# Kernel optimization log

Measured on AMD Instinct MI355X. Metric: run time of the kernel, lower is better.

## Reference

```python
import jax, jax.numpy as jnp
import numpy as np

N_NODES = 100000
N_EDGES = 1600000
D_IN, D_HID, D_OUT = 512, 256, 32


def setup_inputs() -> dict:
    key = jax.random.key(0)
    ks = jax.random.split(key, 8)
    features = jax.random.normal(ks[0], (N_NODES, D_IN), dtype=jnp.float32)
    A_data = jax.random.uniform(ks[1], (N_EDGES,), dtype=jnp.float32)
    A_row = jax.random.randint(ks[2], (N_EDGES,), 0, N_NODES, dtype=jnp.int32)
    A_col = jax.random.randint(ks[3], (N_EDGES,), 0, N_NODES, dtype=jnp.int32)
    # MLP params (glorot-ish scaling)
    W1 = jax.random.normal(ks[4], (D_IN, D_HID), dtype=jnp.float32) * (1.0 / np.sqrt(D_IN))
    b1 = jnp.zeros((D_HID,), dtype=jnp.float32)
    W2 = jax.random.normal(ks[5], (D_HID, D_OUT), dtype=jnp.float32) * (1.0 / np.sqrt(D_HID))
    b2 = jnp.zeros((D_OUT,), dtype=jnp.float32)
    return {"features": features, "A_data": A_data, "W1": W1, "b1": b1,
            "W2": W2, "b2": b2, "A_row": A_row, "A_col": A_col}


def reference(features, A_data, W1, b1, W2, b2, A_row, A_col):
    # head_transform: 2-layer MLP (is_training=False -> dropout identity)
    h = jax.nn.relu(features @ W1 + b1)          # [N, D_HID]
    X = h @ W2 + b2                              # [N, D_OUT]
    # propagator dropout: rate=0.0 / eval mode -> identity on A
    # sparse COO A @ X: gather columns, scale by edge values, scatter-add to rows
    msgs = A_data[:, None] * X[A_col]            # [E, D_OUT]
    out = jax.ops.segment_sum(msgs, A_row, num_segments=N_NODES)  # [N, D_OUT]
    return out
```

## Files before the change

### kernel.cpp

```cpp
#include <hip/hip_runtime.h>
#include <hip/hip_bf16.h>

typedef __bf16 bf16;
typedef __attribute__((ext_vector_type(8))) __bf16 bf16x8;
typedef __attribute__((ext_vector_type(4))) float f32x4;

constexpr int D_IN  = 512;
constexpr int D_HID = 256;
constexpr int D_OUT = 32;
constexpr int BM = 64;
constexpr int BK = 64;
constexpr int HCP = 40;
constexpr int SCAN_VPT  = 8;
constexpr int SCAN_SPAN = 2048;
constexpr int NSLICE = 8;

#define GLOBAL_AS(p) ((const __attribute__((address_space(1))) void*)(p))
#define LDS_AS(p)    ((__attribute__((address_space(3))) void*)(p))

__global__ __launch_bounds__(256) void prep_kernel(
    const float* __restrict__ W1, const float* __restrict__ W2,
    bf16* __restrict__ W1T, bf16* __restrict__ W2T)
{
    int idx = blockIdx.x * 256 + threadIdx.x;
    if (idx < D_IN * D_HID) {
        int k = idx / D_HID, n = idx % D_HID;
        W1T[n * D_IN + k] = (bf16)W1[idx];
    }
    int j = idx - D_IN * D_HID;
    if (j >= 0 && j < D_HID * D_OUT) {
        int k = j / D_OUT, n = j % D_OUT;
        W2T[n * D_HID + k] = (bf16)W2[j];
    }
}

__global__ __launch_bounds__(256) void fused_mlp_kernel(
    const float* __restrict__ feat,
    const bf16* __restrict__ W1T, const bf16* __restrict__ W2T,
    const float* __restrict__ b1, const float* __restrict__ b2,
    float* __restrict__ X, int N)
{
    __shared__ __align__(16) char smem[D_HID * BK * sizeof(bf16)];
    bf16* Bsm = (bf16*)smem;
    bf16* Hc  = (bf16*)smem;

    const int tid  = threadIdx.x;
    const int wave = tid >> 6;
    const int lane = tid & 63;
    const int ln   = lane & 15;
    const int q    = lane >> 4;
    const int mw   = wave * 16;
    const int r0   = blockIdx.x * BM;

    f32x4 acc[16] = {};

    const long arow = (long)min(r0 + mw + ln, N - 1);
    const float* asrc = feat + arow * D_IN + q * 8;

    for (int k0 = 0; k0 < D_IN; k0 += BK) {
        #pragma unroll
        for (int i = 0; i < 8; ++i) {
            int c  = i * 256 + wave * 64 + lane;
            int sl = (c & 7) ^ ((c >> 3) & 7);
            const bf16* gsrc = W1T + ((c >> 3) * D_IN + k0 + sl * 8);
            bf16* lbase = Bsm + (i * 256 + wave * 64) * 8;
            __builtin_amdgcn_global_load_lds(GLOBAL_AS(gsrc), LDS_AS(lbase), 16, 0, 0);
        }

        bf16x8 af0, af1;
        {
            float4 f0 = *(const float4*)(asrc + k0);
            float4 f1 = *(const float4*)(asrc + k0 + 4);
            af0[0] = (bf16)f0.x; af0[1] = (bf16)f0.y; af0[2] = (bf16)f0.z; af0[3] = (bf16)f0.w;
            af0[4] = (bf16)f1.x; af0[5] = (bf16)f1.y; af0[6] = (bf16)f1.z; af0[7] = (bf16)f1.w;
            float4 f2 = *(const float4*)(asrc + k0 + 32);
            float4 f3 = *(const float4*)(asrc + k0 + 36);
            af1[0] = (bf16)f2.x; af1[1] = (bf16)f2.y; af1[2] = (bf16)f2.z; af1[3] = (bf16)f2.w;
            af1[4] = (bf16)f3.x; af1[5] = (bf16)f3.y; af1[6] = (bf16)f3.z; af1[7] = (bf16)f3.w;
        }

        __syncthreads();

        {
            const int psl0 = (0 * 4 + q) ^ (ln & 7);
            #pragma unroll
            for (int t = 0; t < 16; ++t) {
                bf16x8 bfv = *(const bf16x8*)&Bsm[(t * 16 + ln) * BK + psl0 * 8];
                acc[t] = __builtin_amdgcn_mfma_f32_16x16x32_bf16(af0, bfv, acc[t], 0, 0, 0);
            }
            const int psl1 = (1 * 4 + q) ^ (ln & 7);
            #pragma unroll
            for (int t = 0; t < 16; ++t) {
                bf16x8 bfv = *(const bf16x8*)&Bsm[(t * 16 + ln) * BK + psl1 * 8];
                acc[t] = __builtin_amdgcn_mfma_f32_16x16x32_bf16(af1, bfv, acc[t], 0, 0, 0);
            }
        }
        __syncthreads();
    }

    f32x4 acc2[2] = {};
    #pragma unroll
    for (int cc = 0; cc < 8; ++cc) {
        #pragma unroll
        for (int tt = 0; tt < 2; ++tt) {
            int t = cc * 2 + tt;
            float bb = b1[t * 16 + ln];
            #pragma unroll
            for (int i = 0; i < 4; ++i) {
                int row = mw + q * 4 + i;
                float v = acc[t][i] + bb;
                Hc[row * HCP + tt * 16 + ln] = (bf16)fmaxf(v, 0.0f);
            }
        }
        __syncthreads();
        bf16x8 af2 = *(const bf16x8*)&Hc[(mw + ln) * HCP + q * 8];
        int kg = cc * 32 + q * 8;
        #pragma unroll
        for (int t2 = 0; t2 < 2; ++t2) {
            bf16x8 bfv = *(const bf16x8*)&W2T[(t2 * 16 + ln) * D_HID + kg];
            acc2[t2] = __builtin_amdgcn_mfma_f32_16x16x32_bf16(af2, bfv, acc2[t2], 0, 0, 0);
        }
        __syncthreads();
    }

    #pragma unroll
    for (int t = 0; t < 2; ++t) {
        int c = t * 16 + ln;
        float bb = b2[c];
        #pragma unroll
        for (int i = 0; i < 4; ++i) {
            int row = r0 + mw + q * 4 + i;
            if (row < N) X[row * D_OUT + c] = acc2[t][i] + bb;
        }
    }
}

__global__ __launch_bounds__(256) void hist_kernel(
    const int* __restrict__ Arow, int* __restrict__ counts, int E, int rps)
{
    int b = blockIdx.x;
    int slice = b & (NSLICE - 1);
    int e = (b >> 3) * 256 + threadIdx.x;
    if (e >= E) return;
    int r = Arow[e];
    if ((unsigned)(r - slice * rps) >= (unsigned)rps) return;
    atomicAdd(&counts[r], 1);
}

__global__ __launch_bounds__(256) void scanA_kernel(
    const int* __restrict__ counts, int* __restrict__ offs,
    int* __restrict__ partials, int N)
{
    __shared__ int lds[256];
    int t = threadIdx.x;
    int base = blockIdx.x * SCAN_SPAN + t * SCAN_VPT;
    int v[SCAN_VPT];
    int tsum = 0;
    #pragma unroll
    for (int j = 0; j < SCAN_VPT; ++j) {
        v[j] = (base + j < N) ? counts[base + j] : 0;
        tsum += v[j];
    }
    lds[t] = tsum;
    __syncthreads();
    for (int d = 1; d < 256; d <<= 1) {
        int x = (t >= d) ? lds[t - d] : 0;
        __syncthreads();
        lds[t] += x;
        __syncthreads();
    }
    int run = lds[t] - tsum;
    #pragma unroll
    for (int j = 0; j < SCAN_VPT; ++j) {
        if (base + j < N) offs[base + j] = run;
        run += v[j];
    }
    if (t == 255) partials[blockIdx.x] = lds[255];
}

__global__ __launch_bounds__(256) void scanB_kernel(int* __restrict__ partials, int nb)
{
    __shared__ int lds[256];
    int t = threadIdx.x;
    int v = (t < nb) ? partials[t] : 0;
    lds[t] = v;
    __syncthreads();
    for (int d = 1; d < 256; d <<= 1) {
        int x = (t >= d) ? lds[t - d] : 0;
        __syncthreads();
        lds[t] += x;
        __syncthreads();
    }
    if (t < nb) partials[t] = lds[t] - v;
}

__global__ __launch_bounds__(256) void scanC_kernel(
    int* __restrict__ offs, const int* __restrict__ partials,
    int* __restrict__ cursor, int N)
{
    int i = blockIdx.x * 256 + threadIdx.x;
    if (i < N) {
        int o = offs[i] + partials[i / SCAN_SPAN];
        offs[i] = o;
        cursor[i] = o;
    }
}

__global__ __launch_bounds__(256) void reorder_kernel(
    const int* __restrict__ Arow, const int* __restrict__ Acol,
    const float* __restrict__ Adata, int* __restrict__ cursor,
    int2* __restrict__ pairs, int E, int rps)
{
    int b = blockIdx.x;
    int slice = b & (NSLICE - 1);
    int e = (b >> 3) * 256 + threadIdx.x;
    if (e >= E) return;
    int r = Arow[e];
    if ((unsigned)(r - slice * rps) >= (unsigned)rps) return;
    int p = atomicAdd(&cursor[r], 1);
    int2 pk;
    pk.x = Acol[e];
    pk.y = __float_as_int(Adata[e]);
    pairs[p] = pk;
}

__global__ __launch_bounds__(256) void reduce_kernel(
    const int* __restrict__ offs, const int* __restrict__ counts,
    const int2* __restrict__ pairs, const float* __restrict__ X,
    float* __restrict__ out, int N)
{
    int w    = threadIdx.x >> 6;
    int lane = threadIdx.x & 63;
    int r    = blockIdx.x * 4 + w;
    if (r >= N) return;
    int slot = lane >> 3;
    int dg   = lane & 7;
    int off  = offs[r];
    int deg  = counts[r];
    f32x4 acc = {0.0f, 0.0f, 0.0f, 0.0f};
    for (int i = slot; i < deg; i += 8) {
        int2  pk = pairs[off + i];
        float a  = __int_as_float(pk.y);
        f32x4 x  = *(const f32x4*)(X + (long)pk.x * D_OUT + dg * 4);
        acc += a * x;
    }
    #pragma unroll
    for (int d = 8; d < 64; d <<= 1) {
        acc[0] += __shfl_xor(acc[0], d, 64);
        acc[1] += __shfl_xor(acc[1], d, 64);
        acc[2] += __shfl_xor(acc[2], d, 64);
        acc[3] += __shfl_xor(acc[3], d, 64);
    }
    if (slot == 0) *(f32x4*)(out + (long)r * D_OUT + dg * 4) = acc;
}

__global__ __launch_bounds__(256) void scatter_kernel(
    const float* __restrict__ Adata, const int* __restrict__ Arow,
    const int* __restrict__ Acol, const float* __restrict__ X,
    float* __restrict__ out, int E)
{
    int idx = blockIdx.x * 256 + threadIdx.x;
    int e = idx >> 3;
    int g = idx & 7;
    if (e >= E) return;
    int   col = Acol[e];
    int   row = Arow[e];
    float a   = Adata[e];
    float4 x = *(const float4*)(X + (long)col * D_OUT + g * 4);
    float* o = out + (long)row * D_OUT + g * 4;
    unsafeAtomicAdd(o + 0, a * x.x);
    unsafeAtomicAdd(o + 1, a * x.y);
    unsafeAtomicAdd(o + 2, a * x.z);
    unsafeAtomicAdd(o + 3, a * x.w);
}

extern "C" void kernel_launch(void* const* d_in, const int* in_sizes, int n_in,
                              void* d_out, int out_size, void* d_ws, size_t ws_size,
                              hipStream_t stream)
{
    const float* feat  = (const float*)d_in[0];
    const float* Adata = (const float*)d_in[1];
    const float* W1    = (const float*)d_in[2];
    const float* b1    = (const float*)d_in[3];
    const float* W2    = (const float*)d_in[4];
    const float* b2    = (const float*)d_in[5];
    const int*   Arow  = (const int*)d_in[6];
    const int*   Acol  = (const int*)d_in[7];

    const int N = in_sizes[0] / D_IN;
    const int E = in_sizes[1];

    char* p = (char*)d_ws;
    auto alloc = [&](size_t bytes) {
        char* q = p;
        p += (bytes + 255) & ~(size_t)255;
        return q;
    };
    float* X       = (float*)alloc((size_t)N * D_OUT * sizeof(float));
    bf16*  W1T     = (bf16*) alloc((size_t)D_IN * D_HID * sizeof(bf16));
    bf16*  W2T     = (bf16*) alloc((size_t)D_HID * D_OUT * sizeof(bf16));
    int*   counts  = (int*)  alloc((size_t)N * sizeof(int));
    int*   offs    = (int*)  alloc((size_t)N * sizeof(int));
    int*   cursor  = (int*)  alloc((size_t)N * sizeof(int));
    int*   partials= (int*)  alloc(256 * sizeof(int));
    int2*  pairs   = (int2*) alloc((size_t)E * sizeof(int2));
    size_t need = (size_t)(p - (char*)d_ws);
    const bool use_csr = (need <= ws_size);

    float* out = (float*)d_out;

    int prep_elems = D_IN * D_HID + D_HID * D_OUT;
    prep_kernel<<<(prep_elems + 255) / 256, 256, 0, stream>>>(W1, W2, W1T, W2T);

    fused_mlp_kernel<<<(N + BM - 1) / BM, 256, 0, stream>>>(
        feat, W1T, W2T, b1, b2, X, N);

    if (use_csr) {
        hipMemsetAsync(counts, 0, (size_t)N * sizeof(int), stream);
        int rps = (N + NSLICE - 1) / NSLICE;
        hist_kernel<<<NSLICE * ((E + 255) / 256), 256, 0, stream>>>(
            Arow, counts, E, rps);
        int nb = (N + SCAN_SPAN - 1) / SCAN_SPAN;
        scanA_kernel<<<nb, 256, 0, stream>>>(counts, offs, partials, N);
        scanB_kernel<<<1, 256, 0, stream>>>(partials, nb);
        scanC_kernel<<<(N + 255) / 256, 256, 0, stream>>>(offs, partials, cursor, N);
        reorder_kernel<<<NSLICE * ((E + 255) / 256), 256, 0, stream>>>(
            Arow, Acol, Adata, cursor, pairs, E, rps);
        reduce_kernel<<<(N + 3) / 4, 256, 0, stream>>>(
            offs, counts, pairs, X, out, N);
    } else {
        hipMemsetAsync(out, 0, (size_t)out_size * sizeof(float), stream);
        long scatter_threads = (long)E * 8;
        scatter_kernel<<<(scatter_threads + 255) / 256, 256, 0, stream>>>(
            Adata, Arow, Acol, X, out, E);
    }
}
```

Before: 532.5 us.

## Split MLP N-dimension across 8 waves and use grid-stride loops for CSR kernels

The fused MLP kernel now runs 512 threads per block, with two waves per 16-row strip, each owning half of the hidden columns. This halves per-thread accumulators and should lower register pressure, which can raise occupancy. The hist, reorder and reduce kernels switch from one block per chunk to fixed-size grids with grid-stride loops, to cut block launch and scheduling overhead. The risks are more LDS contention and extra barriers in the MLP, plus load imbalance or lost slice/row interleaving in the strided kernels.

```diff
diff --git a/kernel.cpp b/kernel.cpp
--- a/kernel.cpp
+++ b/kernel.cpp
@@ -14,6 +14,7 @@
 constexpr int SCAN_VPT  = 8;
 constexpr int SCAN_SPAN = 2048;
 constexpr int NSLICE = 8;
+constexpr int CHB = 1024;
 
 #define GLOBAL_AS(p) ((const __attribute__((address_space(1))) void*)(p))
 #define LDS_AS(p)    ((__attribute__((address_space(3))) void*)(p))
@@ -34,7 +35,7 @@
     }
 }
 
-__global__ __launch_bounds__(256) void fused_mlp_kernel(
+__global__ __launch_bounds__(512, 4) void fused_mlp_kernel(
     const float* __restrict__ feat,
     const bf16* __restrict__ W1T, const bf16* __restrict__ W2T,
     const float* __restrict__ b1, const float* __restrict__ b2,
@@ -45,25 +46,27 @@
     bf16* Hc  = (bf16*)smem;
 
     const int tid  = threadIdx.x;
-    const int wave = tid >> 6;
+    const int w    = tid >> 6;
     const int lane = tid & 63;
     const int ln   = lane & 15;
     const int q    = lane >> 4;
-    const int mw   = wave * 16;
+    const int s    = w >> 1;
+    const int h    = w & 1;
+    const int mw   = s * 16;
     const int r0   = blockIdx.x * BM;
 
-    f32x4 acc[16] = {};
+    f32x4 acc[8] = {};
 
     const long arow = (long)min(r0 + mw + ln, N - 1);
     const float* asrc = feat + arow * D_IN + q * 8;
 
     for (int k0 = 0; k0 < D_IN; k0 += BK) {
         #pragma unroll
-        for (int i = 0; i < 8; ++i) {
-            int c  = i * 256 + wave * 64 + lane;
+        for (int i = 0; i < 4; ++i) {
+            int c  = i * 512 + w * 64 + lane;
             int sl = (c & 7) ^ ((c >> 3) & 7);
             const bf16* gsrc = W1T + ((c >> 3) * D_IN + k0 + sl * 8);
-            bf16* lbase = Bsm + (i * 256 + wave * 64) * 8;
+            bf16* lbase = Bsm + (i * 512 + w * 64) * 8;
             __builtin_amdgcn_global_load_lds(GLOBAL_AS(gsrc), LDS_AS(lbase), 16, 0, 0);
         }
 
@@ -81,56 +84,55 @@
 
         __syncthreads();
 
-        {
-            const int psl0 = (0 * 4 + q) ^ (ln & 7);
-            #pragma unroll
-            for (int t = 0; t < 16; ++t) {
-                bf16x8 bfv = *(const bf16x8*)&Bsm[(t * 16 + ln) * BK + psl0 * 8];
-                acc[t] = __builtin_amdgcn_mfma_f32_16x16x32_bf16(af0, bfv, acc[t], 0, 0, 0);
-            }
-            const int psl1 = (1 * 4 + q) ^ (ln & 7);
-            #pragma unroll
-            for (int t = 0; t < 16; ++t) {
-                bf16x8 bfv = *(const bf16x8*)&Bsm[(t * 16 + ln) * BK + psl1 * 8];
-                acc[t] = __builtin_amdgcn_mfma_f32_16x16x32_bf16(af1, bfv, acc[t], 0, 0, 0);
-            }
-        }
-        __syncthreads();
-    }
-
-    f32x4 acc2[2] = {};
+        const int psl0 = q ^ (ln & 7);
+        #pragma unroll
+        for (int t = 0; t < 8; ++t) {
+            int row = h * 128 + t * 16 + ln;
+            bf16x8 bfv = *(const bf16x8*)&Bsm[row * BK + psl0 * 8];
+            acc[t] = __builtin_amdgcn_mfma_f32_16x16x32_bf16(af0, bfv, acc[t], 0, 0, 0);
+        }
+        const int psl1 = (4 + q) ^ (ln & 7);
+        #pragma unroll
+        for (int t = 0; t < 8; ++t) {
+            int row = h * 128 + t * 16 + ln;
+            bf16x8 bfv = *(const bf16x8*)&Bsm[row * BK + psl1 * 8];
+            acc[t] = __builtin_amdgcn_mfma_f32_16x16x32_bf16(af1, bfv, acc[t], 0, 0, 0);
+        }
+        __syncthreads();
+    }
+
+    f32x4 acc2 = {};
     #pragma unroll
     for (int cc = 0; cc < 8; ++cc) {
-        #pragma unroll
-        for (int tt = 0; tt < 2; ++tt) {
-            int t = cc * 2 + tt;
-            float bb = b1[t * 16 + ln];
+        if (h == (cc >> 2)) {
             #pragma unroll
-            for (int i = 0; i < 4; ++i) {
-                int row = mw + q * 4 + i;
-                float v = acc[t][i] + bb;
-                Hc[row * HCP + tt * 16 + ln] = (bf16)fmaxf(v, 0.0f);
+            for (int tt = 0; tt < 2; ++tt) {
+                int Tg = cc * 2 + tt;
+                int t  = Tg - h * 8;
+                float bb = b1[Tg * 16 + ln];
+                #pragma unroll
+                for (int i = 0; i < 4; ++i) {
+                    int row = mw + q * 4 + i;
+                    float v = acc[t][i] + bb;
+                    Hc[row * HCP + tt * 16 + ln] = (bf16)fmaxf(v, 0.0f);
+                }
             }
         }
         __syncthreads();
         bf16x8 af2 = *(const bf16x8*)&Hc[(mw + ln) * HCP + q * 8];
         int kg = cc * 32 + q * 8;
-        #pragma unroll
-        for (int t2 = 0; t2 < 2; ++t2) {
-            bf16x8 bfv = *(const bf16x8*)&W2T[(t2 * 16 + ln) * D_HID + kg];
-            acc2[t2] = __builtin_amdgcn_mfma_f32_16x16x32_bf16(af2, bfv, acc2[t2], 0, 0, 0);
-        }
-        __syncthreads();
-    }
-
-    #pragma unroll
-    for (int t = 0; t < 2; ++t) {
-        int c = t * 16 + ln;
+        bf16x8 bfv = *(const bf16x8*)&W2T[(h * 16 + ln) * D_HID + kg];
+        acc2 = __builtin_amdgcn_mfma_f32_16x16x32_bf16(af2, bfv, acc2, 0, 0, 0);
+        __syncthreads();
+    }
+
+    {
+        int c = h * 16 + ln;
         float bb = b2[c];
         #pragma unroll
         for (int i = 0; i < 4; ++i) {
             int row = r0 + mw + q * 4 + i;
-            if (row < N) X[row * D_OUT + c] = acc2[t][i] + bb;
+            if (row < N) X[row * D_OUT + c] = acc2[i] + bb;
         }
     }
 }
@@ -138,13 +140,16 @@
 __global__ __launch_bounds__(256) void hist_kernel(
     const int* __restrict__ Arow, int* __restrict__ counts, int E, int rps)
 {
-    int b = blockIdx.x;
-    int slice = b & (NSLICE - 1);
-    int e = (b >> 3) * 256 + threadIdx.x;
-    if (e >= E) return;
-    int r = Arow[e];
-    if ((unsigned)(r - slice * rps) >= (unsigned)rps) return;
-    atomicAdd(&counts[r], 1);
+    int slice = blockIdx.x & (NSLICE - 1);
+    int nch = (E + 255) / 256;
+    for (int ch = blockIdx.x >> 3; ch < nch; ch += CHB) {
+        int e = ch * 256 + threadIdx.x;
+        if (e < E) {
+            int r = Arow[e];
+            if ((unsigned)(r - slice * rps) < (unsigned)rps)
+                atomicAdd(&counts[r], 1);
+        }
+    }
 }
 
 __global__ __launch_bounds__(256) void scanA_kernel(
@@ -211,47 +216,51 @@
     const float* __restrict__ Adata, int* __restrict__ cursor,
     int2* __restrict__ pairs, int E, int rps)
 {
-    int b = blockIdx.x;
-    int slice = b & (NSLICE - 1);
-    int e = (b >> 3) * 256 + threadIdx.x;
-    if (e >= E) return;
-    int r = Arow[e];
-    if ((unsigned)(r - slice * rps) >= (unsigned)rps) return;
-    int p = atomicAdd(&cursor[r], 1);
-    int2 pk;
-    pk.x = Acol[e];
-    pk.y = __float_as_int(Adata[e]);
-    pairs[p] = pk;
+    int slice = blockIdx.x & (NSLICE - 1);
+    int nch = (E + 255) / 256;
+    for (int ch = blockIdx.x >> 3; ch < nch; ch += CHB) {
+        int e = ch * 256 + threadIdx.x;
+        if (e < E) {
+            int r = Arow[e];
+            if ((unsigned)(r - slice * rps) < (unsigned)rps) {
+                int p = atomicAdd(&cursor[r], 1);
+                int2 pk;
+                pk.x = Acol[e];
+                pk.y = __float_as_int(Adata[e]);
+                pairs[p] = pk;
+            }
+        }
+    }
 }
 
 __global__ __launch_bounds__(256) void reduce_kernel(
     const int* __restrict__ offs, const int* __restrict__ counts,
     const int2* __restrict__ pairs, const float* __restrict__ X,
-    float* __restrict__ out, int N)
+    float* __restrict__ out, int N, int span)
 {
     int w    = threadIdx.x >> 6;
     int lane = threadIdx.x & 63;
-    int r    = blockIdx.x * 4 + w;
-    if (r >= N) return;
     int slot = lane >> 3;
     int dg   = lane & 7;
-    int off  = offs[r];
-    int deg  = counts[r];
-    f32x4 acc = {0.0f, 0.0f, 0.0f, 0.0f};
-    for (int i = slot; i < deg; i += 8) {
-        int2  pk = pairs[off + i];
-        float a  = __int_as_float(pk.y);
-        f32x4 x  = *(const f32x4*)(X + (long)pk.x * D_OUT + dg * 4);
-        acc += a * x;
-    }
-    #pragma unroll
-    for (int d = 8; d < 64; d <<= 1) {
-        acc[0] += __shfl_xor(acc[0], d, 64);
-        acc[1] += __shfl_xor(acc[1], d, 64);
-        acc[2] += __shfl_xor(acc[2], d, 64);
-        acc[3] += __shfl_xor(acc[3], d, 64);
-    }
-    if (slot == 0) *(f32x4*)(out + (long)r * D_OUT + dg * 4) = acc;
+    for (int r = blockIdx.x * 4 + w; r < N; r += span) {
+        int off  = offs[r];
+        int deg  = counts[r];
+        f32x4 acc = {0.0f, 0.0f, 0.0f, 0.0f};
+        for (int i = slot; i < deg; i += 8) {
+            int2  pk = pairs[off + i];
+            float a  = __int_as_float(pk.y);
+            f32x4 x  = *(const f32x4*)(X + (long)pk.x * D_OUT + dg * 4);
+            acc += a * x;
+        }
+        #pragma unroll
+        for (int d = 8; d < 64; d <<= 1) {
+            acc[0] += __shfl_xor(acc[0], d, 64);
+            acc[1] += __shfl_xor(acc[1], d, 64);
+            acc[2] += __shfl_xor(acc[2], d, 64);
+            acc[3] += __shfl_xor(acc[3], d, 64);
+        }
+        if (slot == 0) *(f32x4*)(out + (long)r * D_OUT + dg * 4) = acc;
+    }
 }
 
 __global__ __launch_bounds__(256) void scatter_kernel(
@@ -312,22 +321,22 @@
     int prep_elems = D_IN * D_HID + D_HID * D_OUT;
     prep_kernel<<<(prep_elems + 255) / 256, 256, 0, stream>>>(W1, W2, W1T, W2T);
 
-    fused_mlp_kernel<<<(N + BM - 1) / BM, 256, 0, stream>>>(
+    fused_mlp_kernel<<<(N + BM - 1) / BM, 512, 0, stream>>>(
         feat, W1T, W2T, b1, b2, X, N);
 
     if (use_csr) {
         hipMemsetAsync(counts, 0, (size_t)N * sizeof(int), stream);
         int rps = (N + NSLICE - 1) / NSLICE;
-        hist_kernel<<<NSLICE * ((E + 255) / 256), 256, 0, stream>>>(
-            Arow, counts, E, rps);
+        hist_kernel<<<NSLICE * CHB, 256, 0, stream>>>(Arow, counts, E, rps);
         int nb = (N + SCAN_SPAN - 1) / SCAN_SPAN;
         scanA_kernel<<<nb, 256, 0, stream>>>(counts, offs, partials, N);
         scanB_kernel<<<1, 256, 0, stream>>>(partials, nb);
         scanC_kernel<<<(N + 255) / 256, 256, 0, stream>>>(offs, partials, cursor, N);
-        reorder_kernel<<<NSLICE * ((E + 255) / 256), 256, 0, stream>>>(
+        reorder_kernel<<<NSLICE * CHB, 256, 0, stream>>>(
             Arow, Acol, Adata, cursor, pairs, E, rps);
-        reduce_kernel<<<(N + 3) / 4, 256, 0, stream>>>(
-            offs, counts, pairs, X, out, N);
+        int rblocks = 4096;
+        reduce_kernel<<<rblocks, 256, 0, stream>>>(
+            offs, counts, pairs, X, out, N, rblocks * 4);
     } else {
         hipMemsetAsync(out, 0, (size_t)out_size * sizeof(float), stream);
         long scatter_threads = (long)E * 8;
```

Measured after the change: 548.0 us. 1.03x slower.
